# Optimization experiments

Measured on AMD Instinct MI355X. Metric: run time of the kernel, lower is better.

## Reference

```python
import jax, jax.numpy as jnp
import numpy as np

D_MODEL, N_HEADS, D_HEAD = 1024, 16, 64
BATCH, SEQ = 4, 2048


def setup_inputs() -> dict:
    key = jax.random.key(0)
    ks = jax.random.split(key, 10)
    s = 1.0 / np.sqrt(D_MODEL)
    x = jax.random.normal(ks[0], (BATCH, SEQ, D_MODEL), dtype=jnp.float32)
    attention_mask = jax.random.randint(ks[1], (BATCH, SEQ), 0, 2).astype(jnp.bool_)
    # guarantee at least one attended key per batch row (avoid all -inf softmax)
    attention_mask = attention_mask.at[:, 0].set(True)
    def lin(k):
        kw, kb = jax.random.split(k)
        W = jax.random.uniform(kw, (D_MODEL, D_MODEL), jnp.float32, -s, s)
        b = jax.random.uniform(kb, (D_MODEL,), jnp.float32, -s, s)
        return W, b
    Wq, bq = lin(ks[2]); Wk, bk = lin(ks[3]); Wv, bv = lin(ks[4]); Wo, bo = lin(ks[5])
    return {"x": x, "attention_mask": attention_mask,
            "Wq": Wq, "bq": bq, "Wk": Wk, "bk": bk,
            "Wv": Wv, "bv": bv, "Wo": Wo, "bo": bo}


def reference(x, attention_mask, Wq, bq, Wk, bk, Wv, bv, Wo, bo):
    B, S, _ = x.shape
    def proj(W, b):  # [B,S,d_model] -> [B,S,H,Dh]
        return (x @ W + b).reshape(B, S, N_HEADS, D_HEAD)
    q = proj(Wq, bq)
    k = proj(Wk, bk)
    v = proj(Wv, bv)
    scores = jnp.einsum('bqhd,bkhd->bhqk', q, k)  # [B,H,S,S]
    add_mask = jnp.where(attention_mask, 0.0, jnp.inf)[:, None, None, :]
    # faithful order: subtract mask, THEN scale (inf survives division)
    probs = jax.nn.softmax((scores - add_mask) / jnp.sqrt(jnp.float32(D_HEAD)), axis=-1)
    attn = jnp.einsum('bhqk,bkhd->bqhd', probs, v).reshape(B, S, N_HEADS * D_HEAD)
    return attn @ Wo + bo
```

## Files before the change

### kernel.cpp

```cpp
#include <hip/hip_runtime.h>
#include <math.h>

#define BATCH 4
#define SEQ   2048
#define DM    1024
#define NH    16
#define DH    64
#define MROWS (BATCH * SEQ)

typedef unsigned short ushort_t;
typedef unsigned int   uint_t;
typedef __attribute__((ext_vector_type(8))) short  short8;
typedef __attribute__((ext_vector_type(4))) float  float4v;

__device__ __forceinline__ ushort_t f2bf(float v) {
    uint_t u = __float_as_uint(v);
    u += 0x7FFFu + ((u >> 16) & 1u);
    return (ushort_t)(u >> 16);
}
__device__ __forceinline__ float bf2f(ushort_t h) {
    return __uint_as_float(((uint_t)h) << 16);
}
__device__ __forceinline__ void gload_lds16(const ushort_t* g, ushort_t* lds) {
    __builtin_amdgcn_global_load_lds(
        (const __attribute__((address_space(1))) void*)g,
        (__attribute__((address_space(3))) void*)lds, 16, 0, 0);
}

__global__ __launch_bounds__(256) void conv_x(
    const float* __restrict__ src, ushort_t* __restrict__ dst, int n4)
{
    int i = blockIdx.x * 256 + threadIdx.x;
    if (i >= n4) return;
    float4 v = ((const float4*)src)[i];
    ((ushort4*)dst)[i] = make_ushort4(f2bf(v.x), f2bf(v.y), f2bf(v.z), f2bf(v.w));
}

__global__ __launch_bounds__(256) void convT_w(
    const float* __restrict__ W, ushort_t* __restrict__ ht,
    ushort_t* __restrict__ lt, const int dolo)
{
    __shared__ float sT[64][65];
    const int n0 = blockIdx.x * 64, k0 = blockIdx.y * 64;
    const int t = threadIdx.x;
#pragma unroll
    for (int i = 0; i < 16; i++) {
        int idx = t + i * 256, r = idx >> 6, c = idx & 63;
        sT[r][c] = W[(size_t)(k0 + r) * 1024 + n0 + c];
    }
    __syncthreads();
#pragma unroll
    for (int i = 0; i < 16; i++) {
        int idx = t + i * 256, r = idx >> 6, c = idx & 63;
        float v = sT[c][r];
        ushort_t h = f2bf(v);
        ht[(size_t)(n0 + r) * 1024 + k0 + c] = h;
        if (dolo) lt[(size_t)(n0 + r) * 1024 + k0 + c] = f2bf(v - bf2f(h));
    }
}

__global__ __launch_bounds__(256) void gemm_bf16(
    const ushort_t* __restrict__ A, const ushort_t* __restrict__ Bt,
    const float* __restrict__ bias, const float scale,
    ushort_t* __restrict__ out, const int mode)
{
    __shared__ __align__(16) ushort_t smem[8192];
    const int t = threadIdx.x, lane = t & 63, w = t >> 6;
    const int n0 = blockIdx.x * 128, m0 = blockIdx.y * 128;
    const int wm = (w >> 1) * 64, wn = (w & 1) * 64;
    const int lq = lane >> 4, lc = lane & 15;
    const int gl = (lane & 3) ^ ((lane >> 3) & 3);
    const int irow = lane >> 2;

    float4v acc[4][4];
#pragma unroll
    for (int i = 0; i < 4; i++)
#pragma unroll
        for (int j = 0; j < 4; j++) acc[i][j] = (float4v)(0.0f);

    for (int k0 = 0; k0 < 1024; k0 += 32) {
        __syncthreads();
#pragma unroll
        for (int j = 0; j < 4; j++) {
            const int i = w * 4 + j;
            const ushort_t* src = (i < 8)
                ? A  + (size_t)(m0 + i * 16 + irow) * 1024 + k0 + gl * 8
                : Bt + (size_t)(n0 + (i - 8) * 16 + irow) * 1024 + k0 + gl * 8;
            gload_lds16(src, &smem[i * 512]);
        }
        __syncthreads();

        short8 av[4], bv[4];
#pragma unroll
        for (int mt = 0; mt < 4; mt++) {
            const int r = wm + mt * 16 + lc;
            av[mt] = *(const short8*)&smem[r * 32 + ((lq ^ ((r >> 1) & 3)) * 8)];
        }
#pragma unroll
        for (int nt = 0; nt < 4; nt++) {
            const int r = wn + nt * 16 + lc;
            bv[nt] = *(const short8*)&smem[4096 + r * 32 + ((lq ^ ((r >> 1) & 3)) * 8)];
        }
#pragma unroll
        for (int nt = 0; nt < 4; nt++)
#pragma unroll
            for (int mt = 0; mt < 4; mt++)
                acc[mt][nt] = __builtin_amdgcn_mfma_f32_16x16x32_bf16(av[mt], bv[nt], acc[mt][nt], 0, 0, 0);
    }

#pragma unroll
    for (int nt = 0; nt < 4; nt++) {
        const int n = n0 + wn + nt * 16 + lc;
        const float bvv = bias[n];
        const int h = n >> 6, d = n & 63;
#pragma unroll
        for (int mt = 0; mt < 4; mt++) {
            const int mbase = m0 + wm + mt * 16 + lq * 4;
            const int b = mbase >> 11, s0 = mbase & 2047;
            if (mode == 2) {
                ushort_t hh[4];
#pragma unroll
                for (int r = 0; r < 4; r++) hh[r] = f2bf(acc[mt][nt][r] + bvv);
                *(ushort4*)&out[((size_t)(b * 16 + h) * 64 + d) * 2048 + s0] =
                    make_ushort4(hh[0], hh[1], hh[2], hh[3]);
            } else {
#pragma unroll
                for (int r = 0; r < 4; r++)
                    out[((size_t)(b * 16 + h) * 2048 + s0 + r) * 64 + d] =
                        f2bf((acc[mt][nt][r] + bvv) * scale);
            }
        }
    }
}

__global__ __launch_bounds__(256) void gemm_split3(
    const ushort_t* __restrict__ Ah, const ushort_t* __restrict__ Al,
    const ushort_t* __restrict__ Bh, const ushort_t* __restrict__ Bl,
    const float* __restrict__ bias, float* __restrict__ out)
{
    __shared__ __align__(16) ushort_t smem[16384];
    const int t = threadIdx.x, lane = t & 63, w = t >> 6;
    const int n0 = blockIdx.x * 128, m0 = blockIdx.y * 128;
    const int wm = (w >> 1) * 64, wn = (w & 1) * 64;
    const int lq = lane >> 4, lc = lane & 15;
    const int gl = (lane & 3) ^ ((lane >> 3) & 3);
    const int irow = lane >> 2;

    float4v acc[4][4];
#pragma unroll
    for (int i = 0; i < 4; i++)
#pragma unroll
        for (int j = 0; j < 4; j++) acc[i][j] = (float4v)(0.0f);

    const ushort_t* plane = (w == 0) ? Ah : (w == 1) ? Al : (w == 2) ? Bh : Bl;
    const size_t prow = (size_t)(((w < 2) ? m0 : n0) + irow) * 1024 + gl * 8;

    for (int k0 = 0; k0 < 1024; k0 += 32) {
        __syncthreads();
#pragma unroll
        for (int j = 0; j < 8; j++)
            gload_lds16(plane + prow + (size_t)j * 16384 + k0, &smem[w * 4096 + j * 512]);
        __syncthreads();

        short8 ah[4], al[4];
#pragma unroll
        for (int mt = 0; mt < 4; mt++) {
            const int r = wm + mt * 16 + lc;
            const int off = r * 32 + ((lq ^ ((r >> 1) & 3)) * 8);
            ah[mt] = *(const short8*)&smem[off];
            al[mt] = *(const short8*)&smem[4096 + off];
        }
#pragma unroll
        for (int nt = 0; nt < 4; nt++) {
            const int r = wn + nt * 16 + lc;
            const int off = r * 32 + ((lq ^ ((r >> 1) & 3)) * 8);
            short8 bh = *(const short8*)&smem[8192 + off];
            short8 bl = *(const short8*)&smem[12288 + off];
#pragma unroll
            for (int mt = 0; mt < 4; mt++) {
                acc[mt][nt] = __builtin_amdgcn_mfma_f32_16x16x32_bf16(ah[mt], bh, acc[mt][nt], 0, 0, 0);
                acc[mt][nt] = __builtin_amdgcn_mfma_f32_16x16x32_bf16(al[mt], bh, acc[mt][nt], 0, 0, 0);
                acc[mt][nt] = __builtin_amdgcn_mfma_f32_16x16x32_bf16(ah[mt], bl, acc[mt][nt], 0, 0, 0);
            }
        }
    }

#pragma unroll
    for (int nt = 0; nt < 4; nt++) {
        const int n = n0 + wn + nt * 16 + lc;
        const float bvv = bias[n];
#pragma unroll
        for (int mt = 0; mt < 4; mt++)
#pragma unroll
            for (int r = 0; r < 4; r++) {
                const int m = m0 + wm + mt * 16 + lq * 4 + r;
                out[(size_t)m * 1024 + n] = acc[mt][nt][r] + bvv;
            }
    }
}

__global__ __launch_bounds__(256, 3) void flash_mfma(
    const ushort_t* __restrict__ Q, const ushort_t* __restrict__ K,
    const ushort_t* __restrict__ Vt, const int* __restrict__ mask,
    ushort_t* __restrict__ Oh, ushort_t* __restrict__ Ol)
{
    __shared__ __align__(16) ushort_t smem[26624];
    const int t = threadIdx.x, lane = t & 63, w = t >> 6;
    const int q0 = blockIdx.x * 128;
    const int bh = blockIdx.y, b = bh >> 4, h = bh & 15;
    const int lq = lane >> 4, lc = lane & 15;
    const int wm = w * 32;
    const int gl = (lane & 7) ^ ((lane >> 3) & 7);

    {
        const int4* mrow = (const int4*)(mask + b * SEQ);
        int4 a = mrow[t * 2], c = mrow[t * 2 + 1];
        ((ushort4*)&smem[24576])[t * 2] =
            make_ushort4((ushort_t)a.x, (ushort_t)a.y, (ushort_t)a.z, (ushort_t)a.w);
        ((ushort4*)&smem[24576])[t * 2 + 1] =
            make_ushort4((ushort_t)c.x, (ushort_t)c.y, (ushort_t)c.z, (ushort_t)c.w);
    }
#pragma unroll
    for (int j = 0; j < 4; j++) {
        const int i = w * 4 + j;
        gload_lds16(Q + ((size_t)bh * SEQ + q0 + i * 8 + (lane >> 3)) * 64 + gl * 8,
                    &smem[i * 512]);
    }
    __syncthreads();

    short8 aq[2][2];
#pragma unroll
    for (int mt = 0; mt < 2; mt++)
#pragma unroll
        for (int kk = 0; kk < 2; kk++) {
            const int r = wm + mt * 16 + lc;
            aq[mt][kk] = *(const short8*)&smem[r * 64 + (((kk * 4 + lq) ^ (r & 7)) * 8)];
        }

    float4v O[2][4];
#pragma unroll
    for (int mt = 0; mt < 2; mt++)
#pragma unroll
        for (int nt = 0; nt < 4; nt++) O[mt][nt] = (float4v)(0.0f);
    float li[2] = {0.f, 0.f};

    for (int kt = 0; kt < 32; kt++) {
        const int k0 = kt * 64;
        __syncthreads();
#pragma unroll
        for (int j = 0; j < 4; j++) {
            const int i = w * 4 + j;
            if (i < 8)
                gload_lds16(K + ((size_t)bh * SEQ + k0 + i * 8 + (lane >> 3)) * 64 + gl * 8,
                            &smem[8192 + i * 512]);
            else
                gload_lds16(Vt + ((size_t)bh * 64 + (i - 8) * 8 + (lane >> 3)) * SEQ + k0 + gl * 8,
                            &smem[12288 + (i - 8) * 512]);
        }
        __syncthreads();

        float4v sc[4][2];
#pragma unroll
        for (int kt4 = 0; kt4 < 4; kt4++)
#pragma unroll
            for (int mt = 0; mt < 2; mt++) sc[kt4][mt] = (float4v)(0.0f);
#pragma unroll
        for (int kk = 0; kk < 2; kk++) {
#pragma unroll
            for (int kt4 = 0; kt4 < 4; kt4++) {
                const int kr = kt4 * 16 + lc;
                short8 ak = *(const short8*)&smem[8192 + kr * 64 + (((kk * 4 + lq) ^ (kr & 7)) * 8)];
#pragma unroll
                for (int mt = 0; mt < 2; mt++)
                    sc[kt4][mt] = __builtin_amdgcn_mfma_f32_16x16x32_bf16(ak, aq[mt][kk], sc[kt4][mt], 0, 0, 0);
            }
        }

#pragma unroll
        for (int kt4 = 0; kt4 < 4; kt4++) {
            const ushort4 mv = *(const ushort4*)&smem[24576 + k0 + kt4 * 16 + lq * 4];
#pragma unroll
            for (int mt = 0; mt < 2; mt++) {
                const int qr = wm + mt * 16 + lc;
                uint_t hh[4];
                float ps = 0.f;
                const ushort_t mk[4] = {mv.x, mv.y, mv.z, mv.w};
#pragma unroll
                for (int r = 0; r < 4; r++) {
                    const float p = mk[r] ? __expf(sc[kt4][mt][r]) : 0.0f;
                    const uint_t u = __float_as_uint(p);
                    hh[r] = u >> 16;
                    ps += __uint_as_float(u & 0xFFFF0000u);
                }
                li[mt] += ps;
                *(ushort4*)&smem[16384 + qr * 64 + (((kt4 * 2 + (lq >> 1)) ^ (qr & 7)) * 8) + (lq & 1) * 4] =
                    make_ushort4((ushort_t)hh[0], (ushort_t)hh[1], (ushort_t)hh[2], (ushort_t)hh[3]);
            }
        }

#pragma unroll
        for (int kk = 0; kk < 2; kk++) {
            short8 ap[2];
#pragma unroll
            for (int mt = 0; mt < 2; mt++) {
                const int qr = wm + mt * 16 + lc;
                ap[mt] = *(const short8*)&smem[16384 + qr * 64 + (((kk * 4 + lq) ^ (qr & 7)) * 8)];
            }
#pragma unroll
            for (int nt = 0; nt < 4; nt++) {
                const int d = nt * 16 + lc;
                short8 bv = *(const short8*)&smem[12288 + d * 64 + (((kk * 4 + lq) ^ (d & 7)) * 8)];
#pragma unroll
                for (int mt = 0; mt < 2; mt++)
                    O[mt][nt] = __builtin_amdgcn_mfma_f32_16x16x32_bf16(ap[mt], bv, O[mt][nt], 0, 0, 0);
            }
        }
    }

#pragma unroll
    for (int mt = 0; mt < 2; mt++) {
        li[mt] += __shfl_xor(li[mt], 16);
        li[mt] += __shfl_xor(li[mt], 32);
    }
#pragma unroll
    for (int mt = 0; mt < 2; mt++) {
#pragma unroll
        for (int r = 0; r < 4; r++) {
            const float lsum = __shfl(li[mt], lq * 4 + r);
            const float inv = 1.0f / lsum;
            const int srow = q0 + wm + mt * 16 + lq * 4 + r;
#pragma unroll
            for (int nt = 0; nt < 4; nt++) {
                const float v = O[mt][nt][r] * inv;
                const ushort_t hh = f2bf(v);
                const size_t idx = ((size_t)(b * SEQ + srow)) * 1024 + h * 64 + nt * 16 + lc;
                Oh[idx] = hh;
                Ol[idx] = f2bf(v - bf2f(hh));
            }
        }
    }
}

extern "C" void kernel_launch(void* const* d_in, const int* in_sizes, int n_in,
                              void* d_out, int out_size, void* d_ws, size_t ws_size,
                              hipStream_t stream) {
    const float* x    = (const float*)d_in[0];
    const int*   mask = (const int*)d_in[1];
    const float* Wq   = (const float*)d_in[2];
    const float* bq   = (const float*)d_in[3];
    const float* Wk   = (const float*)d_in[4];
    const float* bk   = (const float*)d_in[5];
    const float* Wv   = (const float*)d_in[6];
    const float* bv   = (const float*)d_in[7];
    const float* Wo   = (const float*)d_in[8];
    const float* bo   = (const float*)d_in[9];
    float* out = (float*)d_out;

    ushort_t* p = (ushort_t*)d_ws;
    const size_t PLANE  = (size_t)MROWS * DM;
    const size_t WPLANE = (size_t)DM * DM;
    ushort_t* xh  = p;  p += PLANE;
    ushort_t* wqh = p;  p += WPLANE;
    ushort_t* wkh = p;  p += WPLANE;
    ushort_t* wvh = p;  p += WPLANE;
    ushort_t* woh = p;  p += WPLANE;
    ushort_t* wol = p;  p += WPLANE;
    ushort_t* Qh  = p;  p += PLANE;
    ushort_t* Kh  = p;  p += PLANE;
    ushort_t* Vth = p;  p += PLANE;
    ushort_t* Ath = p;  p += PLANE;
    ushort_t* Atl = p;  p += PLANE;

    dim3 blk(256);
    hipLaunchKernelGGL(conv_x, dim3(8192), blk, 0, stream, x, xh, 2097152);
    hipLaunchKernelGGL(convT_w, dim3(16, 16), blk, 0, stream, Wq, wqh, (ushort_t*)nullptr, 0);
    hipLaunchKernelGGL(convT_w, dim3(16, 16), blk, 0, stream, Wk, wkh, (ushort_t*)nullptr, 0);
    hipLaunchKernelGGL(convT_w, dim3(16, 16), blk, 0, stream, Wv, wvh, (ushort_t*)nullptr, 0);
    hipLaunchKernelGGL(convT_w, dim3(16, 16), blk, 0, stream, Wo, woh, wol, 1);

    dim3 gemmGrid(8, 64);
    hipLaunchKernelGGL(gemm_bf16, gemmGrid, blk, 0, stream, xh, wqh, bq, 0.125f, Qh, 1);
    hipLaunchKernelGGL(gemm_bf16, gemmGrid, blk, 0, stream, xh, wkh, bk, 1.0f,   Kh, 1);
    hipLaunchKernelGGL(gemm_bf16, gemmGrid, blk, 0, stream, xh, wvh, bv, 1.0f,   Vth, 2);

    hipLaunchKernelGGL(flash_mfma, dim3(16, 64), blk, 0, stream, Qh, Kh, Vth, mask, Ath, Atl);

    hipLaunchKernelGGL(gemm_split3, gemmGrid, blk, 0, stream, Ath, Atl, woh, wol, bo, out);
}
```

Baseline: 372.3 us.

## Fuse QKV projections and weight conversions, fold mask into score bias, shrink flash LDS

```diff
diff --git a/kernel.cpp b/kernel.cpp
--- a/kernel.cpp
+++ b/kernel.cpp
@@ -12,6 +12,8 @@
 typedef unsigned int   uint_t;
 typedef __attribute__((ext_vector_type(8))) short  short8;
 typedef __attribute__((ext_vector_type(4))) float  float4v;
+
+#define QSCALE 0.1803368801111244f
 
 __device__ __forceinline__ ushort_t f2bf(float v) {
     uint_t u = __float_as_uint(v);
@@ -36,11 +38,16 @@
     ((ushort4*)dst)[i] = make_ushort4(f2bf(v.x), f2bf(v.y), f2bf(v.z), f2bf(v.w));
 }
 
-__global__ __launch_bounds__(256) void convT_w(
-    const float* __restrict__ W, ushort_t* __restrict__ ht,
-    ushort_t* __restrict__ lt, const int dolo)
+__global__ __launch_bounds__(256) void convT_w4(
+    const float* __restrict__ W0, const float* __restrict__ W1,
+    const float* __restrict__ W2, const float* __restrict__ W3,
+    ushort_t* __restrict__ fused, ushort_t* __restrict__ woh,
+    ushort_t* __restrict__ wol)
 {
     __shared__ float sT[64][65];
+    const int z = blockIdx.z;
+    const float* W = (z == 0) ? W0 : (z == 1) ? W1 : (z == 2) ? W2 : W3;
+    ushort_t* ht = (z < 3) ? fused + (size_t)z * 1024 * 1024 : woh;
     const int n0 = blockIdx.x * 64, k0 = blockIdx.y * 64;
     const int t = threadIdx.x;
 #pragma unroll
@@ -55,14 +62,16 @@
         float v = sT[c][r];
         ushort_t h = f2bf(v);
         ht[(size_t)(n0 + r) * 1024 + k0 + c] = h;
-        if (dolo) lt[(size_t)(n0 + r) * 1024 + k0 + c] = f2bf(v - bf2f(h));
-    }
-}
-
-__global__ __launch_bounds__(256) void gemm_bf16(
+        if (z == 3) wol[(size_t)(n0 + r) * 1024 + k0 + c] = f2bf(v - bf2f(h));
+    }
+}
+
+__global__ __launch_bounds__(256) void gemm_qkv(
     const ushort_t* __restrict__ A, const ushort_t* __restrict__ Bt,
-    const float* __restrict__ bias, const float scale,
-    ushort_t* __restrict__ out, const int mode)
+    const float* __restrict__ bq, const float* __restrict__ bk,
+    const float* __restrict__ bv,
+    ushort_t* __restrict__ Qh, ushort_t* __restrict__ Kh,
+    ushort_t* __restrict__ Vt)
 {
     __shared__ __align__(16) ushort_t smem[8192];
     const int t = threadIdx.x, lane = t & 63, w = t >> 6;
@@ -71,6 +80,9 @@
     const int lq = lane >> 4, lc = lane & 15;
     const int gl = (lane & 3) ^ ((lane >> 3) & 3);
     const int irow = lane >> 2;
+    const int sect = n0 >> 10;
+    const float* bsel = (sect == 0) ? bq : (sect == 1) ? bk : bv;
+    const float scl = (sect == 0) ? QSCALE : 1.0f;
 
     float4v acc[4][4];
 #pragma unroll
@@ -90,7 +102,7 @@
         }
         __syncthreads();
 
-        short8 av[4], bv[4];
+        short8 av[4], bvf[4];
 #pragma unroll
         for (int mt = 0; mt < 4; mt++) {
             const int r = wm + mt * 16 + lc;
@@ -99,35 +111,36 @@
 #pragma unroll
         for (int nt = 0; nt < 4; nt++) {
             const int r = wn + nt * 16 + lc;
-            bv[nt] = *(const short8*)&smem[4096 + r * 32 + ((lq ^ ((r >> 1) & 3)) * 8)];
+            bvf[nt] = *(const short8*)&smem[4096 + r * 32 + ((lq ^ ((r >> 1) & 3)) * 8)];
         }
 #pragma unroll
         for (int nt = 0; nt < 4; nt++)
 #pragma unroll
             for (int mt = 0; mt < 4; mt++)
-                acc[mt][nt] = __builtin_amdgcn_mfma_f32_16x16x32_bf16(av[mt], bv[nt], acc[mt][nt], 0, 0, 0);
+                acc[mt][nt] = __builtin_amdgcn_mfma_f32_16x16x32_bf16(av[mt], bvf[nt], acc[mt][nt], 0, 0, 0);
     }
 
 #pragma unroll
     for (int nt = 0; nt < 4; nt++) {
-        const int n = n0 + wn + nt * 16 + lc;
-        const float bvv = bias[n];
-        const int h = n >> 6, d = n & 63;
+        const int nn = (n0 + wn + nt * 16 + lc) & 1023;
+        const float bvv = bsel[nn];
+        const int h = nn >> 6, d = nn & 63;
 #pragma unroll
         for (int mt = 0; mt < 4; mt++) {
             const int mbase = m0 + wm + mt * 16 + lq * 4;
             const int b = mbase >> 11, s0 = mbase & 2047;
-            if (mode == 2) {
+            if (sect == 2) {
                 ushort_t hh[4];
 #pragma unroll
                 for (int r = 0; r < 4; r++) hh[r] = f2bf(acc[mt][nt][r] + bvv);
-                *(ushort4*)&out[((size_t)(b * 16 + h) * 64 + d) * 2048 + s0] =
+                *(ushort4*)&Vt[((size_t)(b * 16 + h) * 64 + d) * 2048 + s0] =
                     make_ushort4(hh[0], hh[1], hh[2], hh[3]);
             } else {
+                ushort_t* dst = (sect == 0) ? Qh : Kh;
 #pragma unroll
                 for (int r = 0; r < 4; r++)
-                    out[((size_t)(b * 16 + h) * 2048 + s0 + r) * 64 + d] =
-                        f2bf((acc[mt][nt][r] + bvv) * scale);
+                    dst[((size_t)(b * 16 + h) * 2048 + s0 + r) * 64 + d] =
+                        f2bf((acc[mt][nt][r] + bvv) * scl);
             }
         }
     }
@@ -199,12 +212,12 @@
     }
 }
 
-__global__ __launch_bounds__(256, 3) void flash_mfma(
+__global__ __launch_bounds__(256, 4) void flash_mfma(
     const ushort_t* __restrict__ Q, const ushort_t* __restrict__ K,
     const ushort_t* __restrict__ Vt, const int* __restrict__ mask,
     ushort_t* __restrict__ Oh, ushort_t* __restrict__ Ol)
 {
-    __shared__ __align__(16) ushort_t smem[26624];
+    __shared__ __align__(16) ushort_t smem[18432];
     const int t = threadIdx.x, lane = t & 63, w = t >> 6;
     const int q0 = blockIdx.x * 128;
     const int bh = blockIdx.y, b = bh >> 4, h = bh & 15;
@@ -213,12 +226,13 @@
     const int gl = (lane & 7) ^ ((lane >> 3) & 7);
 
     {
+        const ushort_t NEG = f2bf(-1e30f);
         const int4* mrow = (const int4*)(mask + b * SEQ);
         int4 a = mrow[t * 2], c = mrow[t * 2 + 1];
-        ((ushort4*)&smem[24576])[t * 2] =
-            make_ushort4((ushort_t)a.x, (ushort_t)a.y, (ushort_t)a.z, (ushort_t)a.w);
-        ((ushort4*)&smem[24576])[t * 2 + 1] =
-            make_ushort4((ushort_t)c.x, (ushort_t)c.y, (ushort_t)c.z, (ushort_t)c.w);
+        ((ushort4*)&smem[16384])[t * 2] =
+            make_ushort4(a.x ? 0 : NEG, a.y ? 0 : NEG, a.z ? 0 : NEG, a.w ? 0 : NEG);
+        ((ushort4*)&smem[16384])[t * 2 + 1] =
+            make_ushort4(c.x ? 0 : NEG, c.y ? 0 : NEG, c.z ? 0 : NEG, c.w ? 0 : NEG);
     }
 #pragma unroll
     for (int j = 0; j < 4; j++) {
@@ -259,11 +273,19 @@
         }
         __syncthreads();
 
+        float4v binit[4];
+#pragma unroll
+        for (int kt4 = 0; kt4 < 4; kt4++) {
+            const ushort4 bb = *(const ushort4*)&smem[16384 + k0 + kt4 * 16 + lq * 4];
+            binit[kt4][0] = bf2f(bb.x); binit[kt4][1] = bf2f(bb.y);
+            binit[kt4][2] = bf2f(bb.z); binit[kt4][3] = bf2f(bb.w);
+        }
+
         float4v sc[4][2];
 #pragma unroll
         for (int kt4 = 0; kt4 < 4; kt4++)
 #pragma unroll
-            for (int mt = 0; mt < 2; mt++) sc[kt4][mt] = (float4v)(0.0f);
+            for (int mt = 0; mt < 2; mt++) sc[kt4][mt] = binit[kt4];
 #pragma unroll
         for (int kk = 0; kk < 2; kk++) {
 #pragma unroll
@@ -278,23 +300,23 @@
 
 #pragma unroll
         for (int kt4 = 0; kt4 < 4; kt4++) {
-            const ushort4 mv = *(const ushort4*)&smem[24576 + k0 + kt4 * 16 + lq * 4];
 #pragma unroll
             for (int mt = 0; mt < 2; mt++) {
                 const int qr = wm + mt * 16 + lc;
                 uint_t hh[4];
                 float ps = 0.f;
-                const ushort_t mk[4] = {mv.x, mv.y, mv.z, mv.w};
 #pragma unroll
                 for (int r = 0; r < 4; r++) {
-                    const float p = mk[r] ? __expf(sc[kt4][mt][r]) : 0.0f;
+                    const float p = __builtin_amdgcn_exp2f(sc[kt4][mt][r]);
                     const uint_t u = __float_as_uint(p);
                     hh[r] = u >> 16;
                     ps += __uint_as_float(u & 0xFFFF0000u);
                 }
                 li[mt] += ps;
-                *(ushort4*)&smem[16384 + qr * 64 + (((kt4 * 2 + (lq >> 1)) ^ (qr & 7)) * 8) + (lq & 1) * 4] =
-                    make_ushort4((ushort_t)hh[0], (ushort_t)hh[1], (ushort_t)hh[2], (ushort_t)hh[3]);
+                const uint_t plo = hh[0] | (hh[1] << 16);
+                const uint_t phi = hh[2] | (hh[3] << 16);
+                *(uint2*)&smem[qr * 64 + (((kt4 * 2 + (lq >> 1)) ^ (qr & 7)) * 8) + (lq & 1) * 4] =
+                    make_uint2(plo, phi);
             }
         }
 
@@ -304,7 +326,7 @@
 #pragma unroll
             for (int mt = 0; mt < 2; mt++) {
                 const int qr = wm + mt * 16 + lc;
-                ap[mt] = *(const short8*)&smem[16384 + qr * 64 + (((kk * 4 + lq) ^ (qr & 7)) * 8)];
+                ap[mt] = *(const short8*)&smem[qr * 64 + (((kk * 4 + lq) ^ (qr & 7)) * 8)];
             }
 #pragma unroll
             for (int nt = 0; nt < 4; nt++) {
@@ -360,9 +382,7 @@
     const size_t PLANE  = (size_t)MROWS * DM;
     const size_t WPLANE = (size_t)DM * DM;
     ushort_t* xh  = p;  p += PLANE;
-    ushort_t* wqh = p;  p += WPLANE;
-    ushort_t* wkh = p;  p += WPLANE;
-    ushort_t* wvh = p;  p += WPLANE;
+    ushort_t* wf  = p;  p += 3 * WPLANE;
     ushort_t* woh = p;  p += WPLANE;
     ushort_t* wol = p;  p += WPLANE;
     ushort_t* Qh  = p;  p += PLANE;
@@ -373,17 +393,12 @@
 
     dim3 blk(256);
     hipLaunchKernelGGL(conv_x, dim3(8192), blk, 0, stream, x, xh, 2097152);
-    hipLaunchKernelGGL(convT_w, dim3(16, 16), blk, 0, stream, Wq, wqh, (ushort_t*)nullptr, 0);
-    hipLaunchKernelGGL(convT_w, dim3(16, 16), blk, 0, stream, Wk, wkh, (ushort_t*)nullptr, 0);
-    hipLaunchKernelGGL(convT_w, dim3(16, 16), blk, 0, stream, Wv, wvh, (ushort_t*)nullptr, 0);
-    hipLaunchKernelGGL(convT_w, dim3(16, 16), blk, 0, stream, Wo, woh, wol, 1);
-
-    dim3 gemmGrid(8, 64);
-    hipLaunchKernelGGL(gemm_bf16, gemmGrid, blk, 0, stream, xh, wqh, bq, 0.125f, Qh, 1);
-    hipLaunchKernelGGL(gemm_bf16, gemmGrid, blk, 0, stream, xh, wkh, bk, 1.0f,   Kh, 1);
-    hipLaunchKernelGGL(gemm_bf16, gemmGrid, blk, 0, stream, xh, wvh, bv, 1.0f,   Vth, 2);
-
-    hipLaunchKernelGGL(flash_mfma, dim3(16, 64), blk, 0, stream, Qh, Kh, Vth, mask, Ath, Atl);
-
-    hipLaunchKernelGGL(gemm_split3, gemmGrid, blk, 0, stream, Ath, Atl, woh, wol, bo, out);
-}
+    hipLaunchKernelGGL(convT_w4, dim3(16, 16, 4), blk, 0, stream,
+                       Wq, Wk, Wv, Wo, wf, woh, wol);
+    hipLaunchKernelGGL(gemm_qkv, dim3(24, 64), blk, 0, stream,
+                       xh, wf, bq, bk, bv, Qh, Kh, Vth);
+    hipLaunchKernelGGL(flash_mfma, dim3(16, 64), blk, 0, stream,
+                       Qh, Kh, Vth, mask, Ath, Atl);
+    hipLaunchKernelGGL(gemm_split3, dim3(8, 64), blk, 0, stream,
+                       Ath, Atl, woh, wol, bo, out);
+}
```

Result: faster. 328.0 us (-11.9%).
